# Performance work log

Measured on AMD Instinct MI355X. Metric: run time of the kernel, lower is better.

The kernel has to match this reference:

```python
import jax, jax.numpy as jnp
import numpy as np
import math

B, S, E, H, L, C, DFF = 8, 1024, 512, 8, 2, 8921, 2048
DH = E // H
LN_EPS = 1e-5


def _make_pe(max_len, d):
    pos = np.arange(max_len, dtype=np.float32)[:, None]
    div = np.exp(np.arange(0, d, 2, dtype=np.float32) * (-math.log(10000.0) / d))
    pe = np.zeros((max_len, d), dtype=np.float32)
    pe[:, 0::2] = np.sin(pos * div)
    pe[:, 1::2] = np.cos(pos * div)
    return jnp.asarray(pe)


def setup_inputs() -> dict:
    key = jax.random.key(0)
    ks = jax.random.split(key, 16)
    sc = 0.02
    return {
        'inputs': jax.random.normal(ks[0], (B, S, E), jnp.float32),
        'pe': _make_pe(S, E),
        'label_mat': jax.random.normal(ks[1], (C, E), jnp.float32) * sc,
        'l1_w': jax.random.normal(ks[2], (E, E), jnp.float32) * sc,
        'l1_b': jnp.zeros((E,), jnp.float32),
        'fc_w': jax.random.normal(ks[3], (C, E), jnp.float32) * sc,
        'fc_b': jnp.zeros((C,), jnp.float32),
        'in_proj_w': jax.random.normal(ks[4], (L, 3 * E, E), jnp.float32) * sc,
        'in_proj_b': jnp.zeros((L, 3 * E), jnp.float32),
        'out_proj_w': jax.random.normal(ks[5], (L, E, E), jnp.float32) * sc,
        'out_proj_b': jnp.zeros((L, E), jnp.float32),
        'ln1_w': jnp.ones((L, E), jnp.float32),
        'ln1_b': jnp.zeros((L, E), jnp.float32),
        'ln2_w': jnp.ones((L, E), jnp.float32),
        'ln2_b': jnp.zeros((L, E), jnp.float32),
        'lin1_w': jax.random.normal(ks[6], (L, DFF, E), jnp.float32) * sc,
        'lin1_b': jnp.zeros((L, DFF), jnp.float32),
        'lin2_w': jax.random.normal(ks[7], (L, E, DFF), jnp.float32) * sc,
        'lin2_b': jnp.zeros((L, E), jnp.float32),
    }


def _ln(x, g, b):
    mu = jnp.mean(x, axis=-1, keepdims=True)
    v = jnp.mean(jnp.square(x - mu), axis=-1, keepdims=True)
    return (x - mu) * jax.lax.rsqrt(v + LN_EPS) * g + b


def _encoder_layer(x, wqkv, bqkv, wo, bo, g1, b1, g2, b2, w1, bb1, w2, bb2):
    # x: [B,S,E]; post-norm torch TransformerEncoderLayer with relu
    qkv = x @ wqkv.T + bqkv                      # [B,S,3E]
    q, k, v = jnp.split(qkv, 3, axis=-1)
    q = q.reshape(B, S, H, DH)
    k = k.reshape(B, S, H, DH)
    v = v.reshape(B, S, H, DH)
    scores = jnp.einsum('bqhd,bkhd->bhqk', q, k) / math.sqrt(DH)
    attn = jax.nn.softmax(scores, axis=-1)
    o = jnp.einsum('bhqk,bkhd->bqhd', attn, v).reshape(B, S, E)
    o = o @ wo.T + bo
    x = _ln(x + o, g1, b1)
    ff = jax.nn.relu(x @ w1.T + bb1) @ w2.T + bb2
    return _ln(x + ff, g2, b2)


def reference(inputs, pe, label_mat, l1_w, l1_b, fc_w, fc_b,
              in_proj_w, in_proj_b, out_proj_w, out_proj_b,
              ln1_w, ln1_b, ln2_w, ln2_b,
              lin1_w, lin1_b, lin2_w, lin2_b):
    # faithful to source: pe is indexed by batch position (source bug)
    x = inputs * math.sqrt(E) + pe[:B][:, None, :]      # [B,S,E]
    for i in range(L):
        x = _encoder_layer(x, in_proj_w[i], in_proj_b[i], out_proj_w[i], out_proj_b[i],
                           ln1_w[i], ln1_b[i], ln2_w[i], ln2_b[i],
                           lin1_w[i], lin1_b[i], lin2_w[i], lin2_b[i])
    # label attention
    o1 = jnp.tanh(x @ l1_w.T + l1_b)                    # [B,S,E]
    scores = o1 @ label_mat.T                           # [B,S,C]
    attn_weights = jax.nn.softmax(scores, axis=1)       # over seq dim
    attn_weights = jnp.swapaxes(attn_weights, 1, 2)     # [B,C,S]
    weighted = attn_weights @ x                         # [B,C,E]
    # fused per-class linears: C tiny GEMVs -> one einsum
    outputs = jnp.einsum('bce,ce->bc', weighted, fc_w) + fc_b  # [B,C]
    return outputs, attn_weights
```

## Files before the change

### kernel.cpp

```cpp
#include <hip/hip_runtime.h>
#include <math.h>

#define BB   8
#define SS   1024
#define EE   512
#define HH   8
#define DHH  64
#define LLY  2
#define CC   8921
#define CP   9088
#define DFF_ 2048

typedef short          bf16x8 __attribute__((ext_vector_type(8)));
typedef float          f32x4  __attribute__((ext_vector_type(4)));
typedef unsigned short u16x4  __attribute__((ext_vector_type(4)));
typedef unsigned short u16x8  __attribute__((ext_vector_type(8)));

__device__ __forceinline__ float bf2f(unsigned short u) {
    return __uint_as_float(((unsigned int)u) << 16);
}
__device__ __forceinline__ unsigned short f2bf(float f) {
    unsigned int u = __float_as_uint(f);
    u = (u + 0x7FFFu + ((u >> 16) & 1u)) >> 16;
    return (unsigned short)u;
}
__device__ __forceinline__ void gload16(const void* g, void* l) {
    __builtin_amdgcn_global_load_lds(
        (const __attribute__((address_space(1))) void*)g,
        (__attribute__((address_space(3))) void*)l, 16, 0, 0);
}

__global__ __launch_bounds__(256) void cvt_bf16(const float* __restrict__ in,
                                                unsigned short* __restrict__ out,
                                                long n_in, long n_out)
{
    const long i4 = ((long)blockIdx.x * 256 + threadIdx.x) * 4;
    if (i4 >= n_out) return;
    u16x4 r;
    if (i4 < n_in) {
        const float4 v = *(const float4*)(in + i4);
        r[0] = f2bf(v.x); r[1] = f2bf(v.y); r[2] = f2bf(v.z); r[3] = f2bf(v.w);
    } else {
        r[0] = r[1] = r[2] = r[3] = 0;
    }
    *(u16x4*)(out + i4) = r;
}

__global__ __launch_bounds__(256) void embed_kernel(const float* __restrict__ in,
                                                    const float* __restrict__ pe,
                                                    float* __restrict__ x,
                                                    unsigned short* __restrict__ xb)
{
    const long i  = (long)blockIdx.x * 256 + threadIdx.x;
    const int  e4 = (int)(i & 127);
    const int  b  = (int)(i >> 17);
    float4 v = ((const float4*)in)[i];
    const float4 p = ((const float4*)pe)[b * 128 + e4];
    const float sc = 22.627416997969522f;
    v.x = v.x * sc + p.x;  v.y = v.y * sc + p.y;
    v.z = v.z * sc + p.z;  v.w = v.w * sc + p.w;
    ((float4*)x)[i] = v;
    u16x4 h; h[0] = f2bf(v.x); h[1] = f2bf(v.y); h[2] = f2bf(v.z); h[3] = f2bf(v.w);
    ((u16x4*)xb)[i] = h;
}

template<int FN>
__global__ __launch_bounds__(256) void gemm_mfma_t(const unsigned short* __restrict__ A,
                                                   const unsigned short* __restrict__ B,
                                                   const float* __restrict__ bias,
                                                   float* __restrict__ Cf,
                                                   unsigned short* __restrict__ Ch,
                                                   int M, int N, int K, int Mlim,
                                                   long sAz, long sBz, long sCz,
                                                   int act, int mode)
{
    __shared__ unsigned short As[128 * 64];
    __shared__ unsigned short Bs[32 * FN * 64];
    const int t  = threadIdx.x;
    const int wv = t >> 6, ln = t & 63;
    const int wr = wv >> 1, wc = wv & 1;
    const int lr = ln & 15, lg = ln >> 4;
    const int m0 = blockIdx.x * 128, n0 = blockIdx.y * (32 * FN);
    const int z  = blockIdx.z;
    const unsigned short* Ab = A + (long)z * sAz;
    const unsigned short* Bb = B + (long)z * sBz;

    const int srow = ln >> 3;
    const int ucol = ((ln & 7) ^ srow) << 3;

    f32x4 acc[4][FN];
    #pragma unroll
    for (int i = 0; i < 4; ++i)
        #pragma unroll
        for (int j = 0; j < FN; ++j)
            acc[i][j] = (f32x4){0.f, 0.f, 0.f, 0.f};

    int rA[4], rB[FN];
    #pragma unroll
    for (int f = 0; f < 4; ++f) rA[f] = wr * 64 + f * 16 + lr;
    #pragma unroll
    for (int f = 0; f < FN; ++f) rB[f] = wc * (16 * FN) + f * 16 + lr;

    for (int k0 = 0; k0 < K; k0 += 64) {
        __syncthreads();
        #pragma unroll
        for (int c = 0; c < 4; ++c) {
            const int q   = (wv << 2) + c;
            const int row = (q << 3) + srow;
            gload16(Ab + (long)(m0 + row) * K + k0 + ucol, (char*)As + (q << 10));
        }
        #pragma unroll
        for (int c = 0; c < FN; ++c) {
            const int q   = wv * FN + c;
            const int row = (q << 3) + srow;
            gload16(Bb + (long)(n0 + row) * K + k0 + ucol, (char*)Bs + (q << 10));
        }
        __syncthreads();
        #pragma unroll
        for (int kk = 0; kk < 2; ++kk) {
            bf16x8 af[4], bg[FN];
            const int s = (kk << 2) + lg;
            #pragma unroll
            for (int f = 0; f < 4; ++f)
                af[f] = *(const bf16x8*)((const char*)As + rA[f] * 128 + ((s ^ (rA[f] & 7)) << 4));
            #pragma unroll
            for (int f = 0; f < FN; ++f)
                bg[f] = *(const bf16x8*)((const char*)Bs + rB[f] * 128 + ((s ^ (rB[f] & 7)) << 4));
            #pragma unroll
            for (int i = 0; i < 4; ++i)
                #pragma unroll
                for (int j = 0; j < FN; ++j)
                    acc[i][j] = __builtin_amdgcn_mfma_f32_16x16x32_bf16(af[i], bg[j], acc[i][j], 0, 0, 0);
        }
    }

    const long zC = (long)z * sCz;
    #pragma unroll
    for (int fm = 0; fm < 4; ++fm) {
        #pragma unroll
        for (int reg = 0; reg < 4; ++reg) {
            const int gm = m0 + wr * 64 + fm * 16 + lg * 4 + reg;
            if (gm >= Mlim) continue;
            #pragma unroll
            for (int fn = 0; fn < FN; ++fn) {
                const int gn = n0 + wc * (16 * FN) + fn * 16 + lr;
                float v = acc[fm][fn][reg];
                if (bias) v += bias[gn];
                if (act == 1)      v = fmaxf(v, 0.f);
                else if (act == 2) v = tanhf(v);
                if (mode & 1) Cf[zC + (long)gm * N + gn] = v;
                if (mode & 2) Ch[zC + (long)gm * N + gn] = f2bf(v);
            }
        }
    }
}

__device__ __forceinline__ void label_swizzle(int& bx, int& by, int& bz)
{
    const int flat = blockIdx.x + 71 * (blockIdx.y + 8 * blockIdx.z);
    const int swz  = (flat & 7) * 568 + (flat >> 3);
    bx = swz >> 6;
    by = swz & 7;
    bz = (swz >> 3) & 7;
}

__global__ __launch_bounds__(256) void gemm_scores(const unsigned short* __restrict__ A,
                                                   const unsigned short* __restrict__ B,
                                                   float* __restrict__ attnW,
                                                   float2* __restrict__ stats)
{
    __shared__ unsigned short As[128 * 64];
    __shared__ unsigned short Bs[128 * 64];
    int bx, by, bz;
    label_swizzle(bx, by, bz);
    const int t  = threadIdx.x;
    const int wv = t >> 6, ln = t & 63;
    const int wr = wv >> 1, wc = wv & 1;
    const int lr = ln & 15, lg = ln >> 4;
    const int m0 = bx * 128, n0 = by * 128;
    const int z  = bz;
    const unsigned short* Bb = B + (long)z * SS * EE;

    const int srow = ln >> 3;
    const int ucol = ((ln & 7) ^ srow) << 3;

    f32x4 acc[4][4];
    #pragma unroll
    for (int i = 0; i < 4; ++i)
        #pragma unroll
        for (int j = 0; j < 4; ++j)
            acc[i][j] = (f32x4){0.f, 0.f, 0.f, 0.f};

    int rA[4], rB[4];
    #pragma unroll
    for (int f = 0; f < 4; ++f) {
        rA[f] = wr * 64 + f * 16 + lr;
        rB[f] = wc * 64 + f * 16 + lr;
    }

    for (int k0 = 0; k0 < EE; k0 += 64) {
        __syncthreads();
        #pragma unroll
        for (int c = 0; c < 4; ++c) {
            const int q   = (wv << 2) + c;
            const int row = (q << 3) + srow;
            gload16(A  + (long)(m0 + row) * EE + k0 + ucol, (char*)As + (q << 10));
            gload16(Bb + (long)(n0 + row) * EE + k0 + ucol, (char*)Bs + (q << 10));
        }
        __syncthreads();
        #pragma unroll
        for (int kk = 0; kk < 2; ++kk) {
            bf16x8 af[4], bg[4];
            const int s = (kk << 2) + lg;
            #pragma unroll
            for (int f = 0; f < 4; ++f) {
                af[f] = *(const bf16x8*)((const char*)As + rA[f] * 128 + ((s ^ (rA[f] & 7)) << 4));
                bg[f] = *(const bf16x8*)((const char*)Bs + rB[f] * 128 + ((s ^ (rB[f] & 7)) << 4));
            }
            #pragma unroll
            for (int i = 0; i < 4; ++i)
                #pragma unroll
                for (int j = 0; j < 4; ++j)
                    acc[i][j] = __builtin_amdgcn_mfma_f32_16x16x32_bf16(af[i], bg[j], acc[i][j], 0, 0, 0);
        }
    }

    float* aw = attnW + (long)z * CC * SS;
    #pragma unroll
    for (int fm = 0; fm < 4; ++fm) {
        #pragma unroll
        for (int reg = 0; reg < 4; ++reg) {
            const int r = m0 + wr * 64 + fm * 16 + lg * 4 + reg;
            const float v0 = acc[fm][0][reg], v1 = acc[fm][1][reg];
            const float v2 = acc[fm][2][reg], v3 = acc[fm][3][reg];
            if (r < CC) {
                #pragma unroll
                for (int fn = 0; fn < 4; ++fn) {
                    const int sn = n0 + wc * 64 + fn * 16 + lr;
                    aw[(long)r * SS + sn] = acc[fm][fn][reg];
                }
            }
            float mx = fmaxf(fmaxf(v0, v1), fmaxf(v2, v3));
            mx = fmaxf(mx, __shfl_xor(mx, 1));
            mx = fmaxf(mx, __shfl_xor(mx, 2));
            mx = fmaxf(mx, __shfl_xor(mx, 4));
            mx = fmaxf(mx, __shfl_xor(mx, 8));
            float sm = __expf(v0 - mx) + __expf(v1 - mx) + __expf(v2 - mx) + __expf(v3 - mx);
            sm += __shfl_xor(sm, 1); sm += __shfl_xor(sm, 2);
            sm += __shfl_xor(sm, 4); sm += __shfl_xor(sm, 8);
            if (lr == 0 && r < CC)
                stats[((long)z * CP + r) * 16 + by * 2 + wc] = make_float2(mx, sm);
        }
    }
}

__global__ __launch_bounds__(256) void merge_stats(const float2* __restrict__ stats,
                                                   float2* __restrict__ rowstat)
{
    const long idx = (long)blockIdx.x * 256 + threadIdx.x;
    if (idx >= (long)BB * CP) return;
    const int c = (int)(idx % CP);
    if (c >= CC) return;
    const float2* s = stats + idx * 16;
    float mx = -1e30f;
    #pragma unroll
    for (int i = 0; i < 16; ++i) mx = fmaxf(mx, s[i].x);
    float tot = 0.f;
    #pragma unroll
    for (int i = 0; i < 16; ++i) tot += s[i].y * __expf(s[i].x - mx);
    rowstat[idx] = make_float2(mx, 1.f / tot);
}

__global__ __launch_bounds__(256) void gemm_label_final(const unsigned short* __restrict__ A,
                                                        const unsigned short* __restrict__ B,
                                                        float* __restrict__ attnW,
                                                        const float2* __restrict__ rowstat,
                                                        float* __restrict__ out)
{
    __shared__ unsigned short As[128 * 64];
    __shared__ unsigned short Bs[128 * 64];
    int bx, by, bz;
    label_swizzle(bx, by, bz);
    const int t  = threadIdx.x;
    const int wv = t >> 6, ln = t & 63;
    const int wr = wv >> 1, wc = wv & 1;
    const int lr = ln & 15, lg = ln >> 4;
    const int m0 = bx * 128, n0 = by * 128;
    const int z  = bz;
    const unsigned short* Bb = B + (long)z * SS * EE;

    const int srow = ln >> 3;
    const int ucol = ((ln & 7) ^ srow) << 3;

    f32x4 acc[4][4];
    #pragma unroll
    for (int i = 0; i < 4; ++i)
        #pragma unroll
        for (int j = 0; j < 4; ++j)
            acc[i][j] = (f32x4){0.f, 0.f, 0.f, 0.f};

    int rA[4], rB[4];
    #pragma unroll
    for (int f = 0; f < 4; ++f) {
        rA[f] = wr * 64 + f * 16 + lr;
        rB[f] = wc * 64 + f * 16 + lr;
    }

    for (int k0 = 0; k0 < EE; k0 += 64) {
        __syncthreads();
        #pragma unroll
        for (int c = 0; c < 4; ++c) {
            const int q   = (wv << 2) + c;
            const int row = (q << 3) + srow;
            gload16(A  + (long)(m0 + row) * EE + k0 + ucol, (char*)As + (q << 10));
            gload16(Bb + (long)(n0 + row) * EE + k0 + ucol, (char*)Bs + (q << 10));
        }
        __syncthreads();
        #pragma unroll
        for (int kk = 0; kk < 2; ++kk) {
            bf16x8 af[4], bg[4];
            const int s = (kk << 2) + lg;
            #pragma unroll
            for (int f = 0; f < 4; ++f) {
                af[f] = *(const bf16x8*)((const char*)As + rA[f] * 128 + ((s ^ (rA[f] & 7)) << 4));
                bg[f] = *(const bf16x8*)((const char*)Bs + rB[f] * 128 + ((s ^ (rB[f] & 7)) << 4));
            }
            #pragma unroll
            for (int i = 0; i < 4; ++i)
                #pragma unroll
                for (int j = 0; j < 4; ++j)
                    acc[i][j] = __builtin_amdgcn_mfma_f32_16x16x32_bf16(af[i], bg[j], acc[i][j], 0, 0, 0);
        }
    }

    float* aw = attnW + (long)z * CC * SS;
    const float2* rs = rowstat + (long)z * CP;
    float* outb = out + (long)z * CC;
    #pragma unroll
    for (int fm = 0; fm < 4; ++fm) {
        #pragma unroll
        for (int reg = 0; reg < 4; ++reg) {
            const int r = m0 + wr * 64 + fm * 16 + lg * 4 + reg;
            float pacc = 0.f;
            if (r < CC) {
                const float2 st = rs[r];
                #pragma unroll
                for (int fn = 0; fn < 4; ++fn) {
                    const int sn = n0 + wc * 64 + fn * 16 + lr;
                    const float raw = aw[(long)r * SS + sn];
                    const float p = __expf(raw - st.x) * st.y;
                    aw[(long)r * SS + sn] = p;
                    pacc += p * acc[fm][fn][reg];
                }
            }
            pacc += __shfl_xor(pacc, 1);
            pacc += __shfl_xor(pacc, 2);
            pacc += __shfl_xor(pacc, 4);
            pacc += __shfl_xor(pacc, 8);
            if (lr == 0 && r < CC) atomicAdd(&outb[r], pacc);
        }
    }
}

__global__ __launch_bounds__(256) void vtrans(const unsigned short* __restrict__ qkv,
                                              unsigned short* __restrict__ Vt)
{
    __shared__ unsigned short tile[64][72];
    const int bh = blockIdx.y, b = bh >> 3, h = bh & 7;
    const int s0 = blockIdx.x << 6;
    const int t  = threadIdx.x;
    const int r  = t >> 3;
    const int c8 = (t & 7) << 3;
    const unsigned short* vb = qkv + (long)b * SS * 1536 + 2 * EE + h * DHH;
    #pragma unroll
    for (int rr = 0; rr < 64; rr += 32)
        *(u16x8*)&tile[r + rr][c8] = *(const u16x8*)(vb + (long)(s0 + r + rr) * 1536 + c8);
    __syncthreads();
    #pragma unroll
    for (int rr = 0; rr < 64; rr += 32) {
        const int d = r + rr;
        u16x8 o;
        #pragma unroll
        for (int j = 0; j < 8; ++j) o[j] = tile[c8 + j][d];
        *(u16x8*)(Vt + ((long)bh * DHH + d) * SS + s0 + c8) = o;
    }
}

__global__ __launch_bounds__(256) void flash_mfma(const unsigned short* __restrict__ qkv,
                                                  const unsigned short* __restrict__ Vt,
                                                  unsigned short* __restrict__ o)
{
    __shared__ unsigned short sK[64 * 64];
    __shared__ unsigned short sV[64 * 64];
    __shared__ unsigned short sP[4][16 * 64];
    const int t  = threadIdx.x;
    const int wv = t >> 6, ln = t & 63;
    const int lr = ln & 15, lg = ln >> 4;
    const int bh = blockIdx.y, b = bh >> 3, h = bh & 7;
    const int q0 = (blockIdx.x << 6) + (wv << 4);

    const unsigned short* qb = qkv + (long)b * SS * 1536 + h * DHH;
    const unsigned short* kb = qb + EE;
    const unsigned short* vt = Vt + (long)bh * DHH * SS;
    unsigned short* pw = sP[wv];

    const int srow = ln >> 3;
    const int ucol = ((ln & 7) ^ srow) << 3;

    bf16x8 aq[2];
    #pragma unroll
    for (int c = 0; c < 2; ++c)
        aq[c] = *(const bf16x8*)(qb + (long)(q0 + lr) * 1536 + (c << 5) + (lg << 3));

    float m_[4], l_[4];
    f32x4 accO[4];
    #pragma unroll
    for (int r = 0; r < 4; ++r) { m_[r] = -1e30f; l_[r] = 0.f; }
    #pragma unroll
    for (int n = 0; n < 4; ++n) accO[n] = (f32x4){0.f, 0.f, 0.f, 0.f};

    for (int s0 = 0; s0 < SS; s0 += 64) {
        __syncthreads();
        #pragma unroll
        for (int c = 0; c < 2; ++c) {
            const int row = (wv << 4) + (c << 3) + srow;
            gload16(kb + (long)(s0 + row) * 1536 + ucol, (char*)sK + (((wv << 1) + c) << 10));
            gload16(vt + (long)row * SS + s0 + ucol,     (char*)sV + (((wv << 1) + c) << 10));
        }
        __syncthreads();

        f32x4 accS[4];
        #pragma unroll
        for (int sj = 0; sj < 4; ++sj) accS[sj] = (f32x4){0.f, 0.f, 0.f, 0.f};
        #pragma unroll
        for (int c = 0; c < 2; ++c) {
            const int slot = (c << 2) + lg;
            #pragma unroll
            for (int sj = 0; sj < 4; ++sj) {
                const int rw = (sj << 4) + lr;
                const bf16x8 kf = *(const bf16x8*)((const char*)sK + rw * 128 + ((slot ^ (rw & 7)) << 4));
                accS[sj] = __builtin_amdgcn_mfma_f32_16x16x32_bf16(aq[c], kf, accS[sj], 0, 0, 0);
            }
        }
        #pragma unroll
        for (int reg = 0; reg < 4; ++reg) {
            float sc0 = accS[0][reg] * 0.125f, sc1 = accS[1][reg] * 0.125f;
            float sc2 = accS[2][reg] * 0.125f, sc3 = accS[3][reg] * 0.125f;
            float mx = fmaxf(fmaxf(sc0, sc1), fmaxf(sc2, sc3));
            mx = fmaxf(mx, __shfl_xor(mx, 1));
            mx = fmaxf(mx, __shfl_xor(mx, 2));
            mx = fmaxf(mx, __shfl_xor(mx, 4));
            mx = fmaxf(mx, __shfl_xor(mx, 8));
            const float mnew = fmaxf(m_[reg], mx);
            const float f = __expf(m_[reg] - mnew);
            m_[reg] = mnew;
            sc0 = __expf(sc0 - mnew); sc1 = __expf(sc1 - mnew);
            sc2 = __expf(sc2 - mnew); sc3 = __expf(sc3 - mnew);
            accS[0][reg] = sc0; accS[1][reg] = sc1;
            accS[2][reg] = sc2; accS[3][reg] = sc3;
            float ss = sc0 + sc1 + sc2 + sc3;
            ss += __shfl_xor(ss, 1); ss += __shfl_xor(ss, 2);
            ss += __shfl_xor(ss, 4); ss += __shfl_xor(ss, 8);
            l_[reg] = l_[reg] * f + ss;
            #pragma unroll
            for (int n = 0; n < 4; ++n) accO[n][reg] *= f;
        }
        #pragma unroll
        for (int sj = 0; sj < 4; ++sj) {
            #pragma unroll
            for (int reg = 0; reg < 4; ++reg) {
                const int q = (lg << 2) + reg;
                const int s = (sj << 4) + lr;
                const int byte = (q << 7) + (((s >> 3) ^ (q & 7)) << 4) + ((s & 7) << 1);
                *(unsigned short*)((char*)pw + byte) = f2bf(accS[sj][reg]);
            }
        }
        #pragma unroll
        for (int c2 = 0; c2 < 2; ++c2) {
            const int pslot = ((c2 << 2) + lg) ^ (lr & 7);
            const bf16x8 pa = *(const bf16x8*)((const char*)pw + (lr << 7) + (pslot << 4));
            const int vslot = (c2 << 2) + lg;
            #pragma unroll
            for (int n = 0; n < 4; ++n) {
                const int rw = (n << 4) + lr;
                const bf16x8 vf = *(const bf16x8*)((const char*)sV + rw * 128 + ((vslot ^ (rw & 7)) << 4));
                accO[n] = __builtin_amdgcn_mfma_f32_16x16x32_bf16(pa, vf, accO[n], 0, 0, 0);
            }
        }
    }

    #pragma unroll
    for (int reg = 0; reg < 4; ++reg) {
        const float inv = 1.f / l_[reg];
        unsigned short* orow = o + (long)(b * SS + q0 + (lg << 2) + reg) * EE + h * DHH;
        #pragma unroll
        for (int n = 0; n < 4; ++n)
            orow[(n << 4) + lr] = f2bf(accO[n][reg] * inv);
    }
}

__global__ __launch_bounds__(256) void ln_fused(float* __restrict__ x,
                                                unsigned short* __restrict__ xb,
                                                const float* __restrict__ o,
                                                const float* __restrict__ g,
                                                const float* __restrict__ bta)
{
    const long row = blockIdx.x;
    float* xr = x + row * EE;
    unsigned short* hb = xb + row * EE;
    const float* orr = o + row * EE;
    const int t = threadIdx.x;
    const float v0 = xr[t] + orr[t];
    const float v1 = xr[t + 256] + orr[t + 256];
    float s = v0 + v1;
    #pragma unroll
    for (int off = 1; off < 64; off <<= 1) s += __shfl_xor(s, off);
    __shared__ float r1[4], r2[4];
    if ((t & 63) == 0) r1[t >> 6] = s;
    __syncthreads();
    const float mu = (r1[0] + r1[1] + r1[2] + r1[3]) * (1.f / EE);
    const float d0 = v0 - mu, d1 = v1 - mu;
    float q = d0 * d0 + d1 * d1;
    #pragma unroll
    for (int off = 1; off < 64; off <<= 1) q += __shfl_xor(q, off);
    if ((t & 63) == 0) r2[t >> 6] = q;
    __syncthreads();
    const float rs = rsqrtf((r2[0] + r2[1] + r2[2] + r2[3]) * (1.f / EE) + 1e-5f);
    const float y0 = d0 * rs * g[t]       + bta[t];
    const float y1 = d1 * rs * g[t + 256] + bta[t + 256];
    xr[t] = y0;  xr[t + 256] = y1;
    hb[t] = f2bf(y0);  hb[t + 256] = f2bf(y1);
}

__global__ __launch_bounds__(256) void init_out(float* __restrict__ out,
                                                const float* __restrict__ fcb)
{
    const int i = blockIdx.x * 256 + threadIdx.x;
    if (i < BB * CC) out[i] = fcb[i % CC];
}

extern "C" void kernel_launch(void* const* d_in, const int* in_sizes, int n_in,
                              void* d_out, int out_size, void* d_ws, size_t ws_size,
                              hipStream_t stream)
{
    const float* inp   = (const float*)d_in[0];
    const float* pe    = (const float*)d_in[1];
    const float* label = (const float*)d_in[2];
    const float* l1w   = (const float*)d_in[3];
    const float* l1b   = (const float*)d_in[4];
    const float* fcw   = (const float*)d_in[5];
    const float* fcb   = (const float*)d_in[6];
    const float* ipw   = (const float*)d_in[7];
    const float* ipb   = (const float*)d_in[8];
    const float* opw   = (const float*)d_in[9];
    const float* opb   = (const float*)d_in[10];
    const float* g1    = (const float*)d_in[11];
    const float* b1    = (const float*)d_in[12];
    const float* g2    = (const float*)d_in[13];
    const float* b2    = (const float*)d_in[14];
    const float* w1    = (const float*)d_in[15];
    const float* bb1   = (const float*)d_in[16];
    const float* w2    = (const float*)d_in[17];
    const float* bb2   = (const float*)d_in[18];

    char* wp = (char*)d_ws;
    float* x = (float*)wp;                 wp += (long)BB * SS * EE * 4;
    unsigned short* xb = (unsigned short*)wp;  wp += (long)BB * SS * EE * 2;
    float* bufo = (float*)wp;              wp += (long)BB * SS * EE * 4;
    unsigned short* big = (unsigned short*)wp; wp += (long)BB * SS * DFF_ * 2;
    unsigned short* ob  = (unsigned short*)wp; wp += (long)BB * SS * EE * 2;
    unsigned short* Vtb = (unsigned short*)wp; wp += (long)BB * HH * DHH * SS * 2;
    unsigned short* ipwb = (unsigned short*)wp; wp += (long)LLY * 3 * EE * EE * 2;
    unsigned short* opwb = (unsigned short*)wp; wp += (long)LLY * EE * EE * 2;
    unsigned short* w1b  = (unsigned short*)wp; wp += (long)LLY * DFF_ * EE * 2;
    unsigned short* w2b  = (unsigned short*)wp; wp += (long)LLY * EE * DFF_ * 2;
    unsigned short* l1wb = (unsigned short*)wp; wp += (long)EE * EE * 2;
    unsigned short* labelb = (unsigned short*)wp; wp += (long)CP * EE * 2;
    unsigned short* fcwb   = (unsigned short*)wp; wp += (long)CP * EE * 2;
    float2* stats   = (float2*)wp;         wp += (long)BB * CP * 16 * 8;
    float2* rowstat = (float2*)wp;         wp += (long)BB * CP * 8;

    float* out0  = (float*)d_out;
    float* attnW = out0 + BB * CC;

    {
        const long n1 = (long)LLY * 3 * EE * EE;
        cvt_bf16<<<(int)((n1 / 4 + 255) / 256), 256, 0, stream>>>(ipw, ipwb, n1, n1);
        const long n2 = (long)LLY * EE * EE;
        cvt_bf16<<<(int)((n2 / 4 + 255) / 256), 256, 0, stream>>>(opw, opwb, n2, n2);
        const long n3 = (long)LLY * DFF_ * EE;
        cvt_bf16<<<(int)((n3 / 4 + 255) / 256), 256, 0, stream>>>(w1, w1b, n3, n3);
        cvt_bf16<<<(int)((n3 / 4 + 255) / 256), 256, 0, stream>>>(w2, w2b, n3, n3);
        const long n4 = (long)EE * EE;
        cvt_bf16<<<(int)((n4 / 4 + 255) / 256), 256, 0, stream>>>(l1w, l1wb, n4, n4);
        const long n5i = (long)CC * EE, n5o = (long)CP * EE;
        cvt_bf16<<<(int)((n5o / 4 + 255) / 256), 256, 0, stream>>>(label, labelb, n5i, n5o);
        cvt_bf16<<<(int)((n5o / 4 + 255) / 256), 256, 0, stream>>>(fcw, fcwb, n5i, n5o);
    }

    const int M = BB * SS;

    embed_kernel<<<4096, 256, 0, stream>>>(inp, pe, x, xb);

    for (int l = 0; l < LLY; ++l) {
        gemm_mfma_t<4><<<dim3(64, 12, 1), 256, 0, stream>>>(xb, ipwb + (long)l * 3 * EE * EE,
                                                            ipb + l * 3 * EE, nullptr, big,
                                                            M, 3 * EE, EE, M, 0, 0, 0, 0, 2);
        vtrans<<<dim3(16, 64), 256, 0, stream>>>(big, Vtb);
        flash_mfma<<<dim3(16, 64), 256, 0, stream>>>(big, Vtb, ob);
        gemm_mfma_t<2><<<dim3(64, 8, 1), 256, 0, stream>>>(ob, opwb + (long)l * EE * EE,
                                                           opb + l * EE, bufo, nullptr,
                                                           M, EE, EE, M, 0, 0, 0, 0, 1);
        ln_fused<<<M, 256, 0, stream>>>(x, xb, bufo, g1 + l * EE, b1 + l * EE);
        gemm_mfma_t<4><<<dim3(64, 16, 1), 256, 0, stream>>>(xb, w1b + (long)l * DFF_ * EE,
                                                            bb1 + l * DFF_, nullptr, big,
                                                            M, DFF_, EE, M, 0, 0, 0, 1, 2);
        gemm_mfma_t<2><<<dim3(64, 8, 1), 256, 0, stream>>>(big, w2b + (long)l * EE * DFF_,
                                                           bb2 + l * EE, bufo, nullptr,
                                                           M, EE, DFF_, M, 0, 0, 0, 0, 1);
        ln_fused<<<M, 256, 0, stream>>>(x, xb, bufo, g2 + l * EE, b2 + l * EE);
    }

    gemm_mfma_t<2><<<dim3(64, 8, 1), 256, 0, stream>>>(xb, l1wb, l1b, nullptr, ob,
                                                       M, EE, EE, M, 0, 0, 0, 2, 2);
    gemm_scores<<<dim3(CP / 128, SS / 128, BB), 256, 0, stream>>>(labelb, ob, attnW, stats);
    merge_stats<<<(int)(((long)BB * CP + 255) / 256), 256, 0, stream>>>(stats, rowstat);
    init_out<<<(BB * CC + 255) / 256, 256, 0, stream>>>(out0, fcb);
    gemm_label_final<<<dim3(CP / 128, SS / 128, BB), 256, 0, stream>>>(fcwb, xb, attnW, rowstat, out0);
}
```

Baseline: 1.059 ms.

## Recompute label scores in final kernel instead of storing and rereading raw scores

The scores GEMM now only emits per-row softmax partial stats and no longer writes the raw fp32 score matrix. The final kernel recomputes the scores GEMM, applies the softmax with the merged stats, writes the probabilities once, and then runs the fc_w·x GEMM to form the output. This removes a full fp32 write plus reread of the large [B,C,S] attention tensor (about 290MB each way) at the cost of doing the score GEMM twice. The probabilities used in the output dot product are now bf16-rounded and held in registers, which raises register pressure.

Result: slower. 1.298 ms (+22.5%).

```diff
diff --git a/kernel.cpp b/kernel.cpp
--- a/kernel.cpp
+++ b/kernel.cpp
@@ -164,10 +164,9 @@
     bz = (swz >> 3) & 7;
 }
 
-__global__ __launch_bounds__(256) void gemm_scores(const unsigned short* __restrict__ A,
-                                                   const unsigned short* __restrict__ B,
-                                                   float* __restrict__ attnW,
-                                                   float2* __restrict__ stats)
+__global__ __launch_bounds__(256) void gemm_scores_stats(const unsigned short* __restrict__ A,
+                                                         const unsigned short* __restrict__ B,
+                                                         float2* __restrict__ stats)
 {
     __shared__ unsigned short As[128 * 64];
     __shared__ unsigned short Bs[128 * 64];
@@ -225,7 +224,6 @@
         }
     }
 
-    float* aw = attnW + (long)z * CC * SS;
     #pragma unroll
     for (int fm = 0; fm < 4; ++fm) {
         #pragma unroll
@@ -233,13 +231,6 @@
             const int r = m0 + wr * 64 + fm * 16 + lg * 4 + reg;
             const float v0 = acc[fm][0][reg], v1 = acc[fm][1][reg];
             const float v2 = acc[fm][2][reg], v3 = acc[fm][3][reg];
-            if (r < CC) {
-                #pragma unroll
-                for (int fn = 0; fn < 4; ++fn) {
-                    const int sn = n0 + wc * 64 + fn * 16 + lr;
-                    aw[(long)r * SS + sn] = acc[fm][fn][reg];
-                }
-            }
             float mx = fmaxf(fmaxf(v0, v1), fmaxf(v2, v3));
             mx = fmaxf(mx, __shfl_xor(mx, 1));
             mx = fmaxf(mx, __shfl_xor(mx, 2));
@@ -271,11 +262,13 @@
     rowstat[idx] = make_float2(mx, 1.f / tot);
 }
 
-__global__ __launch_bounds__(256) void gemm_label_final(const unsigned short* __restrict__ A,
-                                                        const unsigned short* __restrict__ B,
-                                                        float* __restrict__ attnW,
-                                                        const float2* __restrict__ rowstat,
-                                                        float* __restrict__ out)
+__global__ __launch_bounds__(256) void gemm_label_final2(const unsigned short* __restrict__ Al,
+                                                         const unsigned short* __restrict__ Bo,
+                                                         const unsigned short* __restrict__ Af,
+                                                         const unsigned short* __restrict__ Bx,
+                                                         float* __restrict__ attnW,
+                                                         const float2* __restrict__ rowstat,
+                                                         float* __restrict__ out)
 {
     __shared__ unsigned short As[128 * 64];
     __shared__ unsigned short Bs[128 * 64];
@@ -287,17 +280,11 @@
     const int lr = ln & 15, lg = ln >> 4;
     const int m0 = bx * 128, n0 = by * 128;
     const int z  = bz;
-    const unsigned short* Bb = B + (long)z * SS * EE;
+    const unsigned short* Bob = Bo + (long)z * SS * EE;
+    const unsigned short* Bxb = Bx + (long)z * SS * EE;
 
     const int srow = ln >> 3;
     const int ucol = ((ln & 7) ^ srow) << 3;
-
-    f32x4 acc[4][4];
-    #pragma unroll
-    for (int i = 0; i < 4; ++i)
-        #pragma unroll
-        for (int j = 0; j < 4; ++j)
-            acc[i][j] = (f32x4){0.f, 0.f, 0.f, 0.f};
 
     int rA[4], rB[4];
     #pragma unroll
@@ -306,14 +293,21 @@
         rB[f] = wc * 64 + f * 16 + lr;
     }
 
+    f32x4 acc[4][4];
+    #pragma unroll
+    for (int i = 0; i < 4; ++i)
+        #pragma unroll
+        for (int j = 0; j < 4; ++j)
+            acc[i][j] = (f32x4){0.f, 0.f, 0.f, 0.f};
+
     for (int k0 = 0; k0 < EE; k0 += 64) {
         __syncthreads();
         #pragma unroll
         for (int c = 0; c < 4; ++c) {
             const int q   = (wv << 2) + c;
             const int row = (q << 3) + srow;
-            gload16(A  + (long)(m0 + row) * EE + k0 + ucol, (char*)As + (q << 10));
-            gload16(Bb + (long)(n0 + row) * EE + k0 + ucol, (char*)Bs + (q << 10));
+            gload16(Al  + (long)(m0 + row) * EE + k0 + ucol, (char*)As + (q << 10));
+            gload16(Bob + (long)(n0 + row) * EE + k0 + ucol, (char*)Bs + (q << 10));
         }
         __syncthreads();
         #pragma unroll
@@ -335,6 +329,59 @@
 
     float* aw = attnW + (long)z * CC * SS;
     const float2* rs = rowstat + (long)z * CP;
+    u16x4 ph[4][4];
+    #pragma unroll
+    for (int fm = 0; fm < 4; ++fm) {
+        #pragma unroll
+        for (int reg = 0; reg < 4; ++reg) {
+            const int r = m0 + wr * 64 + fm * 16 + lg * 4 + reg;
+            float2 st = make_float2(0.f, 0.f);
+            if (r < CC) st = rs[r];
+            #pragma unroll
+            for (int fn = 0; fn < 4; ++fn) {
+                const float p = __expf(acc[fm][fn][reg] - st.x) * st.y;
+                ph[fm][fn][reg] = f2bf(p);
+                if (r < CC) {
+                    const int sn = n0 + wc * 64 + fn * 16 + lr;
+                    aw[(long)r * SS + sn] = p;
+                }
+            }
+        }
+    }
+
+    #pragma unroll
+    for (int i = 0; i < 4; ++i)
+        #pragma unroll
+        for (int j = 0; j < 4; ++j)
+            acc[i][j] = (f32x4){0.f, 0.f, 0.f, 0.f};
+
+    for (int k0 = 0; k0 < EE; k0 += 64) {
+        __syncthreads();
+        #pragma unroll
+        for (int c = 0; c < 4; ++c) {
+            const int q   = (wv << 2) + c;
+            const int row = (q << 3) + srow;
+            gload16(Af  + (long)(m0 + row) * EE + k0 + ucol, (char*)As + (q << 10));
+            gload16(Bxb + (long)(n0 + row) * EE + k0 + ucol, (char*)Bs + (q << 10));
+        }
+        __syncthreads();
+        #pragma unroll
+        for (int kk = 0; kk < 2; ++kk) {
+            bf16x8 af[4], bg[4];
+            const int s = (kk << 2) + lg;
+            #pragma unroll
+            for (int f = 0; f < 4; ++f) {
+                af[f] = *(const bf16x8*)((const char*)As + rA[f] * 128 + ((s ^ (rA[f] & 7)) << 4));
+                bg[f] = *(const bf16x8*)((const char*)Bs + rB[f] * 128 + ((s ^ (rB[f] & 7)) << 4));
+            }
+            #pragma unroll
+            for (int i = 0; i < 4; ++i)
+                #pragma unroll
+                for (int j = 0; j < 4; ++j)
+                    acc[i][j] = __builtin_amdgcn_mfma_f32_16x16x32_bf16(af[i], bg[j], acc[i][j], 0, 0, 0);
+        }
+    }
+
     float* outb = out + (long)z * CC;
     #pragma unroll
     for (int fm = 0; fm < 4; ++fm) {
@@ -342,17 +389,9 @@
         for (int reg = 0; reg < 4; ++reg) {
             const int r = m0 + wr * 64 + fm * 16 + lg * 4 + reg;
             float pacc = 0.f;
-            if (r < CC) {
-                const float2 st = rs[r];
-                #pragma unroll
-                for (int fn = 0; fn < 4; ++fn) {
-                    const int sn = n0 + wc * 64 + fn * 16 + lr;
-                    const float raw = aw[(long)r * SS + sn];
-                    const float p = __expf(raw - st.x) * st.y;
-                    aw[(long)r * SS + sn] = p;
-                    pacc += p * acc[fm][fn][reg];
-                }
-            }
+            #pragma unroll
+            for (int fn = 0; fn < 4; ++fn)
+                pacc += bf2f(ph[fm][fn][reg]) * acc[fm][fn][reg];
             pacc += __shfl_xor(pacc, 1);
             pacc += __shfl_xor(pacc, 2);
             pacc += __shfl_xor(pacc, 4);
@@ -623,8 +662,9 @@
 
     gemm_mfma_t<2><<<dim3(64, 8, 1), 256, 0, stream>>>(xb, l1wb, l1b, nullptr, ob,
                                                        M, EE, EE, M, 0, 0, 0, 2, 2);
-    gemm_scores<<<dim3(CP / 128, SS / 128, BB), 256, 0, stream>>>(labelb, ob, attnW, stats);
+    gemm_scores_stats<<<dim3(CP / 128, SS / 128, BB), 256, 0, stream>>>(labelb, ob, stats);
     merge_stats<<<(int)(((long)BB * CP + 255) / 256), 256, 0, stream>>>(stats, rowstat);
     init_out<<<(BB * CC + 255) / 256, 256, 0, stream>>>(out0, fcb);
-    gemm_label_final<<<dim3(CP / 128, SS / 128, BB), 256, 0, stream>>>(fcwb, xb, attnW, rowstat, out0);
-}
+    gemm_label_final2<<<dim3(CP / 128, SS / 128, BB), 256, 0, stream>>>(labelb, ob, fcwb, xb,
+                                                                        attnW, rowstat, out0);
+}
```
